# Kernel tuning notes

Measured on AMD Instinct MI355X. Metric: run time of the kernel, lower is better.

Reference implementation:

```python
import jax, jax.numpy as jnp
import numpy as np

N_NODES = 100000


def gcn_conv(x, edge_index, W, b, n_nodes):
    """PyG GCNConv: out = D^-1/2 (A + I) D^-1/2 (x @ W^T) + b."""
    src, dst = edge_index[0], edge_index[1]
    loop = jnp.arange(n_nodes, dtype=src.dtype)
    src = jnp.concatenate([src, loop])  # [E + N]
    dst = jnp.concatenate([dst, loop])
    # degree of each node as aggregation target (includes self loop)
    deg = jax.ops.segment_sum(jnp.ones_like(src, dtype=x.dtype), dst,
                              num_segments=n_nodes)
    deg_inv_sqrt = jnp.where(deg > 0, jax.lax.rsqrt(deg), 0.0)
    norm = deg_inv_sqrt[src] * deg_inv_sqrt[dst]  # [E + N]
    h = x @ W.T  # [N, out_dim]  (transform BEFORE propagate, as in PyG)
    msg = h[src] * norm[:, None]  # gather + scale  [E + N, out_dim]
    out = jax.ops.segment_sum(msg, dst, num_segments=n_nodes)  # scatter-add
    return out + b


def setup_inputs() -> dict:
    key = jax.random.key(0)
    k_x, k_e, k_w1, k_b1, k_w2, k_b2 = jax.random.split(key, 6)
    in_dim, hidden = 128, 16
    n_edges = 3200000
    x = jax.random.normal(k_x, (N_NODES, in_dim), dtype=jnp.float32)
    edge_index = jax.random.randint(k_e, (2, n_edges), 0, N_NODES,
                                    dtype=jnp.int64)
    # Glorot-ish init for the linear weights (PyG Linear stores [out, in])
    W1 = jax.random.normal(k_w1, (hidden, in_dim), dtype=jnp.float32) / np.sqrt(in_dim)
    b1 = jnp.zeros((hidden,), dtype=jnp.float32)
    W2 = jax.random.normal(k_w2, (1, hidden), dtype=jnp.float32) / np.sqrt(hidden)
    b2 = jnp.zeros((1,), dtype=jnp.float32)
    return {"x": x, "edge_index": edge_index,
            "W1": W1, "b1": b1, "W2": W2, "b2": b2}


def reference(x, edge_index, W1, b1, W2, b2):
    n = x.shape[0]
    h = jax.nn.relu(gcn_conv(x, edge_index, W1, b1, n))  # [N, hidden]
    out = gcn_conv(h, edge_index, W2, b2, n)  # [N, 1]
    return out.squeeze(-1)  # [N]
```

## Files before the change

kernel.cpp:

```cpp
#include <hip/hip_runtime.h>

#define IN_DIM 128
#define HID 16
#define BSHIFT 8
#define BMASK  255
#define BCAP   9216
#define MID    4608
#define PCH    8192
#define PTHR   512
#define EPT    (PCH / PTHR)
#define TSCALE 4096.0f
#define ZSCALE 262144.0f

__global__ void init_kernel(const unsigned int* ei, int* flag, int* gcur) {
    int tid = blockIdx.x * blockDim.x + threadIdx.x;
    if (tid < 4096) gcur[tid] = 0;
    if (tid == 0) {
        int zeros = 0;
        for (int j = 0; j < 8; ++j)
            if (ei[2 * j + 1] == 0u) zeros++;
        *flag = (zeros >= 7) ? 1 : 0;
    }
}

__device__ __forceinline__ int edge_at(const void* ei, long long idx, int is64) {
    if (is64) return (int)((const long long*)ei)[idx];
    return ((const int*)ei)[idx];
}

__global__ __launch_bounds__(PTHR) void place_kernel(const void* ei, long long E,
        int* gcur, unsigned int* __restrict__ binned, int NB, const int* flag) {
    __shared__ int cnt[1024];
    __shared__ int wbase[1024];
    int tid = threadIdx.x;
    for (int i = tid; i < NB; i += PTHR) cnt[i] = 0;
    __syncthreads();
    const int is64 = *flag;
    const long long e0 = (long long)blockIdx.x * PCH;

    int sA[EPT], dA[EPT];
    if (e0 + PCH <= E) {
        if (is64) {
            const long long* p = (const long long*)ei;
#pragma unroll
            for (int j = 0; j < EPT; ++j) sA[j] = (int)p[e0 + j * PTHR + tid];
#pragma unroll
            for (int j = 0; j < EPT; ++j) dA[j] = (int)p[E + e0 + j * PTHR + tid];
        } else {
            const int* p = (const int*)ei;
#pragma unroll
            for (int j = 0; j < EPT; ++j) sA[j] = p[e0 + j * PTHR + tid];
#pragma unroll
            for (int j = 0; j < EPT; ++j) dA[j] = p[E + e0 + j * PTHR + tid];
        }
    } else {
#pragma unroll
        for (int j = 0; j < EPT; ++j) {
            long long e = e0 + j * PTHR + tid;
            bool ok = e < E;
            sA[j] = ok ? edge_at(ei, e, is64) : 0;
            dA[j] = ok ? edge_at(ei, E + e, is64) : -(BMASK + 1);
        }
    }

    unsigned int v[EPT];
    unsigned int br[EPT];
#pragma unroll
    for (int j = 0; j < EPT; ++j) {
        int b = dA[j] >> BSHIFT;
        bool ok = dA[j] >= 0;
        int r = ok ? atomicAdd(&cnt[b], 1) : 0;
        v[j]  = ((unsigned int)sA[j] << BSHIFT) | (unsigned int)(dA[j] & BMASK);
        br[j] = ok ? (((unsigned int)b << 16) | (unsigned int)r) : 0xFFFFFFFFu;
    }
    __syncthreads();
    const int q = (int)(blockIdx.x & 3);
    int* gc = gcur + q * 1024;
    for (int i = tid; i < NB; i += PTHR) {
        int c = cnt[i];
        wbase[i] = c ? atomicAdd(&gc[i], c) : 0;
    }
    __syncthreads();
    const int regBase = (q >> 1) * MID;
    const bool down = (q & 1);
#pragma unroll
    for (int j = 0; j < EPT; ++j) {
        if (br[j] != 0xFFFFFFFFu) {
            int b = (int)(br[j] >> 16);
            int r = (int)(br[j] & 0xFFFFu);
            int w = wbase[b] + r;
            if (w < MID) {
                int pos = regBase + (down ? (MID - 1 - w) : w);
                binned[(size_t)b * BCAP + pos] = v[j];
            }
        }
    }
}

__device__ __forceinline__ void bucket_ranges(const int* gcur, int b,
        int& r0hi, int& r1lo, int& r1hi, int& r2lo) {
    int cA = gcur[b];            if (cA > MID) cA = MID;
    int cB = gcur[1024 + b];     if (cB > MID - cA) cB = MID - cA;
    int cC = gcur[2048 + b];     if (cC > MID) cC = MID;
    int cD = gcur[3072 + b];     if (cD > MID - cC) cD = MID - cC;
    r0hi = cA;
    r1lo = MID - cB;
    r1hi = MID + cC;
    r2lo = BCAP - cD;
}

__global__ __launch_bounds__(1024) void disgemm_kernel(
        const unsigned int* __restrict__ binned, const int* __restrict__ gcur,
        const float* __restrict__ x, const float* __restrict__ W1,
        float* __restrict__ dis, short* __restrict__ ts16, int N) {
    __shared__ float red[4 * 256 * 17];
    __shared__ int cnt[256];
    __shared__ float disl[256];
    int b = blockIdx.x, tid = threadIdx.x;
    int base = b * BCAP;
    int r0hi, r1lo, r1hi, r2lo;
    bucket_ranges(gcur, b, r0hi, r1lo, r1hi, r2lo);

    if (tid < 256) cnt[tid] = 0;
    __syncthreads();
    for (int e = tid; e < r0hi; e += 1024)
        atomicAdd(&cnt[binned[(size_t)base + e] & BMASK], 1);
    for (int e = r1lo + tid; e < r1hi; e += 1024)
        atomicAdd(&cnt[binned[(size_t)base + e] & BMASK], 1);
    for (int e = r2lo + tid; e < BCAP; e += 1024)
        atomicAdd(&cnt[binned[(size_t)base + e] & BMASK], 1);
    __syncthreads();
    if (tid < 256) {
        float dv = rsqrtf((float)(cnt[tid] + 1));
        disl[tid] = dv;
        int node = (b << BSHIFT) + tid;
        if (node < N) dis[node] = dv;
    }
    __syncthreads();

    {
        const int wq = __builtin_amdgcn_readfirstlane(tid >> 8);
        const int nl = tid & 255;
        const int node = (b << BSHIFT) + nl;
        float acc[HID];
#pragma unroll
        for (int o = 0; o < HID; ++o) acc[o] = 0.f;
        if (node < N) {
            const float* xp = &x[(size_t)node * IN_DIM + wq * 32];
            float4 xv[8];
#pragma unroll
            for (int j = 0; j < 8; ++j) xv[j] = ((const float4*)xp)[j];
            const float* wp = &W1[wq * 32];
#pragma unroll
            for (int kk = 0; kk < 32; ++kk) {
                float xs = ((const float*)xv)[kk];
#pragma unroll
                for (int o = 0; o < HID; ++o)
                    acc[o] = fmaf(xs, wp[(size_t)o * IN_DIM + kk], acc[o]);
            }
        }
#pragma unroll
        for (int o = 0; o < HID; ++o)
            red[((size_t)wq * 256 + nl) * 17 + o] = acc[o];
    }
    __syncthreads();
    {
        const int nl = tid >> 2;
        const int og = (tid & 3) * 4;
        const int node = (b << BSHIFT) + nl;
        if (node < N) {
            float s0 = 0.f, s1 = 0.f, s2 = 0.f, s3 = 0.f;
#pragma unroll
            for (int w2 = 0; w2 < 4; ++w2) {
                const float* rp = &red[((size_t)w2 * 256 + nl) * 17 + og];
                s0 += rp[0]; s1 += rp[1]; s2 += rp[2]; s3 += rp[3];
            }
            float di = disl[nl] * TSCALE;
            int i0 = (int)rintf(fminf(fmaxf(di * s0, -32767.f), 32767.f));
            int i1 = (int)rintf(fminf(fmaxf(di * s1, -32767.f), 32767.f));
            int i2 = (int)rintf(fminf(fmaxf(di * s2, -32767.f), 32767.f));
            int i3 = (int)rintf(fminf(fmaxf(di * s3, -32767.f), 32767.f));
            uint2 pk;
            pk.x = ((unsigned int)i0 & 0xFFFFu) | ((unsigned int)i1 << 16);
            pk.y = ((unsigned int)i2 & 0xFFFFu) | ((unsigned int)i3 << 16);
            ((uint2*)ts16)[(size_t)node * 4 + (tid & 3)] = pk;
        }
    }
}

__global__ __launch_bounds__(1024) void agg1_kernel(
        const unsigned int* __restrict__ binned, const int* __restrict__ gcur,
        const short* __restrict__ ts16, const float* __restrict__ dis,
        const float* __restrict__ b1, const float* __restrict__ W2,
        float* __restrict__ zs, int N) {
    __shared__ int acc[256 * 17];
    int b = blockIdx.x, tid = threadIdx.x;
    for (int i = tid; i < 256 * 17; i += 1024) acc[i] = 0;
    __syncthreads();
    int base = b * BCAP;
    int r0hi, r1lo, r1hi, r2lo;
    bucket_ranges(gcur, b, r0hi, r1lo, r1hi, r2lo);

#define AGG1_EDGE(IDX)                                                        \
    {                                                                         \
        unsigned int v = binned[(size_t)base + (IDX)];                        \
        int src = (int)(v >> BSHIFT);                                         \
        int row = (int)(v & BMASK) * 17;                                      \
        const int4* tp = (const int4*)(ts16 + (size_t)src * 16);              \
        int4 a = tp[0], c = tp[1];                                            \
        atomicAdd(&acc[row + 0],  (int)(short)(a.x & 0xFFFF));                \
        atomicAdd(&acc[row + 1],  a.x >> 16);                                 \
        atomicAdd(&acc[row + 2],  (int)(short)(a.y & 0xFFFF));                \
        atomicAdd(&acc[row + 3],  a.y >> 16);                                 \
        atomicAdd(&acc[row + 4],  (int)(short)(a.z & 0xFFFF));                \
        atomicAdd(&acc[row + 5],  a.z >> 16);                                 \
        atomicAdd(&acc[row + 6],  (int)(short)(a.w & 0xFFFF));                \
        atomicAdd(&acc[row + 7],  a.w >> 16);                                 \
        atomicAdd(&acc[row + 8],  (int)(short)(c.x & 0xFFFF));                \
        atomicAdd(&acc[row + 9],  c.x >> 16);                                 \
        atomicAdd(&acc[row + 10], (int)(short)(c.y & 0xFFFF));                \
        atomicAdd(&acc[row + 11], c.y >> 16);                                 \
        atomicAdd(&acc[row + 12], (int)(short)(c.z & 0xFFFF));                \
        atomicAdd(&acc[row + 13], c.z >> 16);                                 \
        atomicAdd(&acc[row + 14], (int)(short)(c.w & 0xFFFF));                \
        atomicAdd(&acc[row + 15], c.w >> 16);                                 \
    }

    for (int e = tid; e < r0hi; e += 1024) AGG1_EDGE(e)
    for (int e = r1lo + tid; e < r1hi; e += 1024) AGG1_EDGE(e)
    for (int e = r2lo + tid; e < BCAP; e += 1024) AGG1_EDGE(e)
#undef AGG1_EDGE
    __syncthreads();
    if (tid < 256) {
        int node = (b << BSHIFT) + tid;
        if (node < N) {
            float di = dis[tid + (b << BSHIFT)];
            const int4* tp = (const int4*)(ts16 + (size_t)node * 16);
            int4 a = tp[0], c = tp[1];
            int self[16] = {
                (int)(short)(a.x & 0xFFFF), a.x >> 16,
                (int)(short)(a.y & 0xFFFF), a.y >> 16,
                (int)(short)(a.z & 0xFFFF), a.z >> 16,
                (int)(short)(a.w & 0xFFFF), a.w >> 16,
                (int)(short)(c.x & 0xFFFF), c.x >> 16,
                (int)(short)(c.y & 0xFFFF), c.y >> 16,
                (int)(short)(c.z & 0xFFFF), c.z >> 16,
                (int)(short)(c.w & 0xFFFF), c.w >> 16 };
            float z = 0.f;
#pragma unroll
            for (int j = 0; j < 16; ++j) {
                float s = (float)(acc[tid * 17 + j] + self[j]) * (1.0f / TSCALE);
                float h = fmaxf(fmaf(di, s, b1[j]), 0.f);
                z = fmaf(h, W2[j], z);
            }
            zs[node] = di * z;
        }
    }
}

__global__ __launch_bounds__(1024) void agg2_kernel(
        const unsigned int* __restrict__ binned, const int* __restrict__ gcur,
        const float* __restrict__ zs, const float* __restrict__ dis,
        const float* __restrict__ b2, float* __restrict__ out, int N) {
    __shared__ int acc2[256];
    int b = blockIdx.x, tid = threadIdx.x;
    if (tid < 256) acc2[tid] = 0;
    __syncthreads();
    int base = b * BCAP;
    int r0hi, r1lo, r1hi, r2lo;
    bucket_ranges(gcur, b, r0hi, r1lo, r1hi, r2lo);
    for (int e = tid; e < r0hi; e += 1024) {
        unsigned int v = binned[(size_t)base + e];
        atomicAdd(&acc2[v & BMASK], (int)rintf(zs[v >> BSHIFT] * ZSCALE));
    }
    for (int e = r1lo + tid; e < r1hi; e += 1024) {
        unsigned int v = binned[(size_t)base + e];
        atomicAdd(&acc2[v & BMASK], (int)rintf(zs[v >> BSHIFT] * ZSCALE));
    }
    for (int e = r2lo + tid; e < BCAP; e += 1024) {
        unsigned int v = binned[(size_t)base + e];
        atomicAdd(&acc2[v & BMASK], (int)rintf(zs[v >> BSHIFT] * ZSCALE));
    }
    __syncthreads();
    if (tid < 256) {
        int node = (b << BSHIFT) + tid;
        if (node < N) {
            float s = (float)acc2[tid] * (1.0f / ZSCALE) + zs[node];
            out[node] = fmaf(dis[node], s, b2[0]);
        }
    }
}

extern "C" void kernel_launch(void* const* d_in, const int* in_sizes, int n_in,
                              void* d_out, int out_size, void* d_ws, size_t ws_size,
                              hipStream_t stream) {
    const float* x  = (const float*)d_in[0];
    const void*  ei = d_in[1];
    const float* W1 = (const float*)d_in[2];
    const float* b1 = (const float*)d_in[3];
    const float* W2 = (const float*)d_in[4];
    const float* b2 = (const float*)d_in[5];
    float* out = (float*)d_out;

    const int N = in_sizes[0] / IN_DIM;
    const long long E = in_sizes[1] / 2;
    const int NB = (N + BMASK) >> BSHIFT;

    char* w = (char*)d_ws;
    unsigned int* binned = (unsigned int*)w;  w += (size_t)NB * BCAP * sizeof(unsigned int);
    short* ts16   = (short*)w;  w += (size_t)N * HID * sizeof(short);
    float* zs     = (float*)w;  w += (size_t)N * sizeof(float);
    float* dis    = (float*)w;  w += (size_t)N * sizeof(float);
    int*   gcur   = (int*)w;    w += 4096 * sizeof(int);
    int*   flag   = (int*)w;

    init_kernel<<<16, 256, 0, stream>>>((const unsigned int*)ei, flag, gcur);

    int pblk = (int)((E + PCH - 1) / PCH);
    place_kernel<<<pblk, PTHR, 0, stream>>>(ei, E, gcur, binned, NB, flag);

    disgemm_kernel<<<NB, 1024, 0, stream>>>(binned, gcur, x, W1, dis, ts16, N);

    agg1_kernel<<<NB, 1024, 0, stream>>>(binned, gcur, ts16, dis, b1, W2, zs, N);

    agg2_kernel<<<NB, 1024, 0, stream>>>(binned, gcur, zs, dis, b2, out, N);
}
```

Baseline: 99.60 us.

## Overlap x@W1 GEMM with edge binning in one fused launch

Moves the dense x@W1 transform out of the degree kernel and into extra blocks of the edge-placement launch, so the GEMM runs concurrently with the scatter into bins. The GEMM stores unscaled int16 values, and the degree kernel then rescales them in place by deg^-1/2. This is meant to hide the GEMM's memory traffic behind the bandwidth-bound placement phase and shorten the degree kernel. In exchange it adds a second rounding step, which changes numerics slightly, plus an extra read and write pass over ts16.

Measured after the change: 92.62 us. 1.08x faster.

```diff
diff --git a/kernel.cpp b/kernel.cpp
--- a/kernel.cpp
+++ b/kernel.cpp
@@ -7,8 +7,8 @@
 #define BCAP   9216
 #define MID    4608
 #define PCH    8192
-#define PTHR   512
-#define EPT    (PCH / PTHR)
+#define FTHR   512
+#define EPT    (PCH / FTHR)
 #define TSCALE 4096.0f
 #define ZSCALE 262144.0f
 
@@ -28,71 +28,125 @@
     return ((const int*)ei)[idx];
 }
 
-__global__ __launch_bounds__(PTHR) void place_kernel(const void* ei, long long E,
-        int* gcur, unsigned int* __restrict__ binned, int NB, const int* flag) {
-    __shared__ int cnt[1024];
-    __shared__ int wbase[1024];
+__global__ __launch_bounds__(FTHR) void fat_kernel(const void* ei, long long E,
+        int* gcur, unsigned int* __restrict__ binned, int NB, const int* flag,
+        const float* __restrict__ x, const float* __restrict__ W1,
+        short* __restrict__ ts16, int N, int pblk) {
+    __shared__ float smem[4 * 128 * 17];
     int tid = threadIdx.x;
-    for (int i = tid; i < NB; i += PTHR) cnt[i] = 0;
-    __syncthreads();
-    const int is64 = *flag;
-    const long long e0 = (long long)blockIdx.x * PCH;
-
-    int sA[EPT], dA[EPT];
-    if (e0 + PCH <= E) {
-        if (is64) {
-            const long long* p = (const long long*)ei;
-#pragma unroll
-            for (int j = 0; j < EPT; ++j) sA[j] = (int)p[e0 + j * PTHR + tid];
-#pragma unroll
-            for (int j = 0; j < EPT; ++j) dA[j] = (int)p[E + e0 + j * PTHR + tid];
+    if ((int)blockIdx.x < pblk) {
+        int* cnt = (int*)smem;
+        int* wbase = cnt + 1024;
+        for (int i = tid; i < NB; i += FTHR) cnt[i] = 0;
+        __syncthreads();
+        const int is64 = *flag;
+        const long long e0 = (long long)blockIdx.x * PCH;
+
+        int sA[EPT], dA[EPT];
+        if (e0 + PCH <= E) {
+            if (is64) {
+                const long long* p = (const long long*)ei;
+#pragma unroll
+                for (int j = 0; j < EPT; ++j) sA[j] = (int)p[e0 + j * FTHR + tid];
+#pragma unroll
+                for (int j = 0; j < EPT; ++j) dA[j] = (int)p[E + e0 + j * FTHR + tid];
+            } else {
+                const int* p = (const int*)ei;
+#pragma unroll
+                for (int j = 0; j < EPT; ++j) sA[j] = p[e0 + j * FTHR + tid];
+#pragma unroll
+                for (int j = 0; j < EPT; ++j) dA[j] = p[E + e0 + j * FTHR + tid];
+            }
         } else {
-            const int* p = (const int*)ei;
-#pragma unroll
-            for (int j = 0; j < EPT; ++j) sA[j] = p[e0 + j * PTHR + tid];
-#pragma unroll
-            for (int j = 0; j < EPT; ++j) dA[j] = p[E + e0 + j * PTHR + tid];
+#pragma unroll
+            for (int j = 0; j < EPT; ++j) {
+                long long e = e0 + j * FTHR + tid;
+                bool ok = e < E;
+                sA[j] = ok ? edge_at(ei, e, is64) : 0;
+                dA[j] = ok ? edge_at(ei, E + e, is64) : -(BMASK + 1);
+            }
+        }
+
+        unsigned int v[EPT];
+        unsigned int br[EPT];
+#pragma unroll
+        for (int j = 0; j < EPT; ++j) {
+            int b = dA[j] >> BSHIFT;
+            bool ok = dA[j] >= 0;
+            int r = ok ? atomicAdd(&cnt[b], 1) : 0;
+            v[j]  = ((unsigned int)sA[j] << BSHIFT) | (unsigned int)(dA[j] & BMASK);
+            br[j] = ok ? (((unsigned int)b << 16) | (unsigned int)r) : 0xFFFFFFFFu;
+        }
+        __syncthreads();
+        const int q = (int)(blockIdx.x & 3);
+        int* gc = gcur + q * 1024;
+        for (int i = tid; i < NB; i += FTHR) {
+            int c = cnt[i];
+            wbase[i] = c ? atomicAdd(&gc[i], c) : 0;
+        }
+        __syncthreads();
+        const int regBase = (q >> 1) * MID;
+        const bool down = (q & 1);
+#pragma unroll
+        for (int j = 0; j < EPT; ++j) {
+            if (br[j] != 0xFFFFFFFFu) {
+                int b = (int)(br[j] >> 16);
+                int r = (int)(br[j] & 0xFFFFu);
+                int w = wbase[b] + r;
+                if (w < MID) {
+                    int pos = regBase + (down ? (MID - 1 - w) : w);
+                    binned[(size_t)b * BCAP + pos] = v[j];
+                }
+            }
         }
     } else {
-#pragma unroll
-        for (int j = 0; j < EPT; ++j) {
-            long long e = e0 + j * PTHR + tid;
-            bool ok = e < E;
-            sA[j] = ok ? edge_at(ei, e, is64) : 0;
-            dA[j] = ok ? edge_at(ei, E + e, is64) : -(BMASK + 1);
-        }
-    }
-
-    unsigned int v[EPT];
-    unsigned int br[EPT];
-#pragma unroll
-    for (int j = 0; j < EPT; ++j) {
-        int b = dA[j] >> BSHIFT;
-        bool ok = dA[j] >= 0;
-        int r = ok ? atomicAdd(&cnt[b], 1) : 0;
-        v[j]  = ((unsigned int)sA[j] << BSHIFT) | (unsigned int)(dA[j] & BMASK);
-        br[j] = ok ? (((unsigned int)b << 16) | (unsigned int)r) : 0xFFFFFFFFu;
-    }
-    __syncthreads();
-    const int q = (int)(blockIdx.x & 3);
-    int* gc = gcur + q * 1024;
-    for (int i = tid; i < NB; i += PTHR) {
-        int c = cnt[i];
-        wbase[i] = c ? atomicAdd(&gc[i], c) : 0;
-    }
-    __syncthreads();
-    const int regBase = (q >> 1) * MID;
-    const bool down = (q & 1);
-#pragma unroll
-    for (int j = 0; j < EPT; ++j) {
-        if (br[j] != 0xFFFFFFFFu) {
-            int b = (int)(br[j] >> 16);
-            int r = (int)(br[j] & 0xFFFFu);
-            int w = wbase[b] + r;
-            if (w < MID) {
-                int pos = regBase + (down ? (MID - 1 - w) : w);
-                binned[(size_t)b * BCAP + pos] = v[j];
-            }
+        const int nb = (int)blockIdx.x - pblk;
+        const int lane = tid & 63;
+        const int kq = __builtin_amdgcn_readfirstlane(tid >> 7);
+        const int half = (tid >> 6) & 1;
+        const int nl = half * 64 + lane;
+        const int node = nb * 128 + nl;
+
+        float acc[HID];
+#pragma unroll
+        for (int o = 0; o < HID; ++o) acc[o] = 0.f;
+        if (node < N) {
+            const float* xp = &x[(size_t)node * IN_DIM + kq * 32];
+            float4 xv[8];
+#pragma unroll
+            for (int j = 0; j < 8; ++j) xv[j] = ((const float4*)xp)[j];
+            const float* wp = &W1[kq * 32];
+#pragma unroll
+            for (int kk = 0; kk < 32; ++kk) {
+                float xs = ((const float*)xv)[kk];
+#pragma unroll
+                for (int o = 0; o < HID; ++o)
+                    acc[o] = fmaf(xs, wp[(size_t)o * IN_DIM + kk], acc[o]);
+            }
+        }
+#pragma unroll
+        for (int o = 0; o < HID; ++o)
+            smem[((size_t)kq * 128 + nl) * 17 + o] = acc[o];
+        __syncthreads();
+
+        const int nl2 = tid >> 2;
+        const int og = (tid & 3) * 4;
+        const int node2 = nb * 128 + nl2;
+        if (node2 < N) {
+            float s0 = 0.f, s1 = 0.f, s2 = 0.f, s3 = 0.f;
+#pragma unroll
+            for (int w2 = 0; w2 < 4; ++w2) {
+                const float* rp = &smem[((size_t)w2 * 128 + nl2) * 17 + og];
+                s0 += rp[0]; s1 += rp[1]; s2 += rp[2]; s3 += rp[3];
+            }
+            int i0 = (int)rintf(fminf(fmaxf(TSCALE * s0, -32767.f), 32767.f));
+            int i1 = (int)rintf(fminf(fmaxf(TSCALE * s1, -32767.f), 32767.f));
+            int i2 = (int)rintf(fminf(fmaxf(TSCALE * s2, -32767.f), 32767.f));
+            int i3 = (int)rintf(fminf(fmaxf(TSCALE * s3, -32767.f), 32767.f));
+            uint2 pk;
+            pk.x = ((unsigned int)i0 & 0xFFFFu) | ((unsigned int)i1 << 16);
+            pk.y = ((unsigned int)i2 & 0xFFFFu) | ((unsigned int)i3 << 16);
+            ((uint2*)ts16)[(size_t)node2 * 4 + (tid & 3)] = pk;
         }
     }
 }
@@ -109,18 +163,15 @@
     r2lo = BCAP - cD;
 }
 
-__global__ __launch_bounds__(1024) void disgemm_kernel(
+__global__ __launch_bounds__(1024) void degdis_kernel(
         const unsigned int* __restrict__ binned, const int* __restrict__ gcur,
-        const float* __restrict__ x, const float* __restrict__ W1,
         float* __restrict__ dis, short* __restrict__ ts16, int N) {
-    __shared__ float red[4 * 256 * 17];
     __shared__ int cnt[256];
     __shared__ float disl[256];
     int b = blockIdx.x, tid = threadIdx.x;
     int base = b * BCAP;
     int r0hi, r1lo, r1hi, r2lo;
     bucket_ranges(gcur, b, r0hi, r1lo, r1hi, r2lo);
-
     if (tid < 256) cnt[tid] = 0;
     __syncthreads();
     for (int e = tid; e < r0hi; e += 1024)
@@ -137,53 +188,24 @@
         if (node < N) dis[node] = dv;
     }
     __syncthreads();
-
     {
-        const int wq = __builtin_amdgcn_readfirstlane(tid >> 8);
-        const int nl = tid & 255;
-        const int node = (b << BSHIFT) + nl;
-        float acc[HID];
-#pragma unroll
-        for (int o = 0; o < HID; ++o) acc[o] = 0.f;
+        int nl = tid >> 2, part = tid & 3;
+        int node = (b << BSHIFT) + nl;
         if (node < N) {
-            const float* xp = &x[(size_t)node * IN_DIM + wq * 32];
-            float4 xv[8];
-#pragma unroll
-            for (int j = 0; j < 8; ++j) xv[j] = ((const float4*)xp)[j];
-            const float* wp = &W1[wq * 32];
-#pragma unroll
-            for (int kk = 0; kk < 32; ++kk) {
-                float xs = ((const float*)xv)[kk];
-#pragma unroll
-                for (int o = 0; o < HID; ++o)
-                    acc[o] = fmaf(xs, wp[(size_t)o * IN_DIM + kk], acc[o]);
-            }
-        }
-#pragma unroll
-        for (int o = 0; o < HID; ++o)
-            red[((size_t)wq * 256 + nl) * 17 + o] = acc[o];
-    }
-    __syncthreads();
-    {
-        const int nl = tid >> 2;
-        const int og = (tid & 3) * 4;
-        const int node = (b << BSHIFT) + nl;
-        if (node < N) {
-            float s0 = 0.f, s1 = 0.f, s2 = 0.f, s3 = 0.f;
-#pragma unroll
-            for (int w2 = 0; w2 < 4; ++w2) {
-                const float* rp = &red[((size_t)w2 * 256 + nl) * 17 + og];
-                s0 += rp[0]; s1 += rp[1]; s2 += rp[2]; s3 += rp[3];
-            }
-            float di = disl[nl] * TSCALE;
-            int i0 = (int)rintf(fminf(fmaxf(di * s0, -32767.f), 32767.f));
-            int i1 = (int)rintf(fminf(fmaxf(di * s1, -32767.f), 32767.f));
-            int i2 = (int)rintf(fminf(fmaxf(di * s2, -32767.f), 32767.f));
-            int i3 = (int)rintf(fminf(fmaxf(di * s3, -32767.f), 32767.f));
-            uint2 pk;
-            pk.x = ((unsigned int)i0 & 0xFFFFu) | ((unsigned int)i1 << 16);
-            pk.y = ((unsigned int)i2 & 0xFFFFu) | ((unsigned int)i3 << 16);
-            ((uint2*)ts16)[(size_t)node * 4 + (tid & 3)] = pk;
+            uint2 v = ((uint2*)ts16)[(size_t)node * 4 + part];
+            float dv = disl[nl];
+            int a0 = (int)(short)(v.x & 0xFFFF);
+            int a1 = (int)v.x >> 16;
+            int a2 = (int)(short)(v.y & 0xFFFF);
+            int a3 = (int)v.y >> 16;
+            int r0 = (int)rintf((float)a0 * dv);
+            int r1 = (int)rintf((float)a1 * dv);
+            int r2 = (int)rintf((float)a2 * dv);
+            int r3 = (int)rintf((float)a3 * dv);
+            uint2 o;
+            o.x = ((unsigned int)r0 & 0xFFFFu) | ((unsigned int)r1 << 16);
+            o.y = ((unsigned int)r2 & 0xFFFFu) | ((unsigned int)r3 << 16);
+            ((uint2*)ts16)[(size_t)node * 4 + part] = o;
         }
     }
 }
@@ -234,7 +256,7 @@
     if (tid < 256) {
         int node = (b << BSHIFT) + tid;
         if (node < N) {
-            float di = dis[tid + (b << BSHIFT)];
+            float di = dis[node];
             const int4* tp = (const int4*)(ts16 + (size_t)node * 16);
             int4 a = tp[0], c = tp[1];
             int self[16] = {
@@ -317,9 +339,11 @@
     init_kernel<<<16, 256, 0, stream>>>((const unsigned int*)ei, flag, gcur);
 
     int pblk = (int)((E + PCH - 1) / PCH);
-    place_kernel<<<pblk, PTHR, 0, stream>>>(ei, E, gcur, binned, NB, flag);
-
-    disgemm_kernel<<<NB, 1024, 0, stream>>>(binned, gcur, x, W1, dis, ts16, N);
+    int gblk = (N + 127) / 128;
+    fat_kernel<<<pblk + gblk, FTHR, 0, stream>>>(
+        ei, E, gcur, binned, NB, flag, x, W1, ts16, N, pblk);
+
+    degdis_kernel<<<NB, 1024, 0, stream>>>(binned, gcur, dis, ts16, N);
 
     agg1_kernel<<<NB, 1024, 0, stream>>>(binned, gcur, ts16, dis, b1, W2, zs, N);
 
```
